# Kernel optimization log

Measured on AMD Instinct MI355X. Metric: run time of the kernel, lower is better.

Reference implementation:

```python
import jax, jax.numpy as jnp
import numpy as np

EPS = 1e-3  # denominator regularizer for weighted mean/cov
DIST_SCALE = 10.0  # raw_call applies 10.0 * distsq before exp weighting

V, K, C, F = 100000, 40, 3, 32


def setup_inputs() -> dict:
    key = jax.random.key(0)
    k1, k2, k3, k4 = jax.random.split(key, 4)
    coordinates = jax.random.normal(k1, (V, C), dtype=jnp.float32)
    distsq = jax.random.uniform(k2, (V, K), dtype=jnp.float32)  # squared distances >= 0
    features = jax.random.uniform(k3, (V, F), dtype=jnp.float32)  # non-negative activations
    n_idxs = jax.random.randint(k4, (V, K), 0, V, dtype=jnp.int32)
    return {"coordinates": coordinates, "distsq": distsq, "features": features, "n_idxs": n_idxs}


def reference(coordinates, distsq, features, n_idxs):
    nV, nC = coordinates.shape
    nF = features.shape[1]
    # SelectWithDefault semantics: index -1 -> default 0
    valid = (n_idxs >= 0)
    idx = jnp.where(valid, n_idxs, 0)
    n_coords = jnp.where(valid[..., None], coordinates[idx], 0.0)  # V x K x C
    w = jnp.exp(-DIST_SCALE * distsq)  # V x K distance weights
    n_feat = jnp.where(valid[..., None], features[idx], 0.0) * w[..., None]  # V x K x F (feature weights)
    wsum = jnp.sum(n_feat, axis=1)  # V x F
    denom = wsum[:, :, None] + EPS  # V x F x 1
    # weighted first moment -> means, weighted second moment -> covariance
    means = jnp.einsum('vkf,vkc->vfc', n_feat, n_coords) / denom  # V x F x C
    second = jnp.einsum('vkf,vkc,vkd->vfcd', n_feat, n_coords, n_coords) / denom[..., None]  # V x F x C x C
    cov = second - means[:, :, :, None] * means[:, :, None, :]  # centered covariance
    out = jnp.concatenate([cov.reshape(nV, nF * nC * nC), means.reshape(nV, nF * nC)], axis=-1)
    return out
```

## Files before the change

### kernel.cpp

```cpp
#include <hip/hip_runtime.h>


constexpr int K = 40;
constexpr int C = 3;
constexpr int F = 32;
constexpr int FH = 16;
constexpr float EPS = 1e-3f;
constexpr float DIST_SCALE = 10.0f;
constexpr int OUT_PER_V = F * C * C + F * C;
constexpr int VPB = 16;
constexpr int PAIRS = VPB * K;
constexpr int WSTRIDE = K + 1;
constexpr int STAGE_F4 = VPB * 48;

typedef float    floatx4 __attribute__((ext_vector_type(4)));
typedef float    f32x8   __attribute__((ext_vector_type(8)));
typedef _Float16 f16x8   __attribute__((ext_vector_type(8)));

__global__ __launch_bounds__(256) void cvt_kernel(
    const float* __restrict__ in, _Float16* __restrict__ lo,
    _Float16* __restrict__ hi, int n4)
{
    const int i = blockIdx.x * 256 + threadIdx.x;
    if (i >= n4) return;
    const int v = i >> 2, q = i & 3;
    const f32x8 x = __builtin_nontemporal_load((const f32x8*)in + i);
    const f16x8 o = __builtin_convertvector(x, f16x8);
    _Float16* dst = (q < 2 ? lo : hi) + (size_t)v * FH + (q & 1) * 8;
    *(f16x8*)dst = o;
}

__global__ __launch_bounds__(256) void neighcov_split(
    const float* __restrict__ coords,
    const float* __restrict__ distsq,
    const _Float16* __restrict__ plane_lo,
    const _Float16* __restrict__ plane_hi,
    const int*   __restrict__ nidx,
    float* __restrict__ out,
    int V)
{
    __shared__ float4  s_wxyz[VPB * WSTRIDE];
    __shared__ int     s_joff[PAIRS];
    __shared__ floatx4 s_stage[STAGE_F4];

    const int tid   = threadIdx.x;
    const int vbase = blockIdx.x * VPB;
    const long long total_pairs = (long long)V * K;

    for (int p = tid; p < PAIRS; p += 256) {
        const long long gp = (long long)vbase * K + p;
        int idx = -1;
        float d = 0.f;
        if (gp < total_pairs) {
            idx = __builtin_nontemporal_load(nidx + gp);
            d   = __builtin_nontemporal_load(distsq + gp);
        }
        const bool valid = (idx >= 0);
        const int j = valid ? idx : 0;
        const float w = valid ? __expf(-DIST_SCALE * d) : 0.f;
        const float x = coords[(size_t)j * 3 + 0];
        const float y = coords[(size_t)j * 3 + 1];
        const float z = coords[(size_t)j * 3 + 2];
        const int vloc = p / K, k = p - vloc * K;
        s_wxyz[vloc * WSTRIDE + k] = make_float4(w, x, y, z);
        s_joff[p] = j * FH;
    }
    __syncthreads();

    const int fl   = tid & 15;
    const int vloc = tid >> 4;
    const float4* wp = &s_wxyz[vloc * WSTRIDE];
    const int*    jp = &s_joff[vloc * K];
    const int rem_v = V - vbase;
    floatx4* o4 = (floatx4*)(out + (size_t)vbase * OUT_PER_V);

    #pragma unroll
    for (int half = 0; half < 2; ++half) {
        const _Float16* __restrict__ plane = half ? plane_hi : plane_lo;

        float wsum = 0.f;
        float m0 = 0.f, m1 = 0.f, m2 = 0.f;
        float s00 = 0.f, s01 = 0.f, s02 = 0.f, s11 = 0.f, s12 = 0.f, s22 = 0.f;

        #pragma unroll 8
        for (int k = 0; k < K; ++k) {
            const float4 q = wp[k];
            const int jo   = jp[k];
            const float feat = (float)plane[jo + fl];
            const float fw = q.x * feat;
            const float x = q.y, y = q.z, z = q.w;
            const float fx = fw * x, fy = fw * y, fz = fw * z;
            wsum += fw;
            m0 += fx;        m1 += fy;        m2 += fz;
            s00 += fx * x;   s01 += fx * y;   s02 += fx * z;
            s11 += fy * y;   s12 += fy * z;   s22 += fz * z;
        }

        const float inv = 1.f / (wsum + EPS);
        const float mu0 = m0 * inv, mu1 = m1 * inv, mu2 = m2 * inv;
        const float c00 = s00 * inv - mu0 * mu0;
        const float c01 = s01 * inv - mu0 * mu1;
        const float c02 = s02 * inv - mu0 * mu2;
        const float c11 = s11 * inv - mu1 * mu1;
        const float c12 = s12 * inv - mu1 * mu2;
        const float c22 = s22 * inv - mu2 * mu2;

        float* s_out = (float*)s_stage;
        float* so = s_out + vloc * 192 + fl * 9;
        so[0] = c00; so[1] = c01; so[2] = c02;
        so[3] = c01; so[4] = c11; so[5] = c12;
        so[6] = c02; so[7] = c12; so[8] = c22;
        float* sm = s_out + vloc * 192 + 144 + fl * 3;
        sm[0] = mu0; sm[1] = mu1; sm[2] = mu2;

        __syncthreads();

        #pragma unroll
        for (int g = tid; g < STAGE_F4; g += 256) {
            const int v = g / 48;
            const int r = g - v * 48;
            if (v < rem_v) {
                const int dst = v * 96 + (r < 36 ? half * 36 + r
                                                 : 72 + half * 12 + (r - 36));
                __builtin_nontemporal_store(s_stage[g], o4 + dst);
            }
        }

        __syncthreads();
    }
}

constexpr int VPB8 = 8;
constexpr int PAIRS8 = VPB8 * K;
constexpr int OUT_F4_8 = VPB8 * OUT_PER_V / 4;

__global__ __launch_bounds__(256) void neighcov_f32(
    const float* __restrict__ coords, const float* __restrict__ distsq,
    const float* __restrict__ features, const int* __restrict__ nidx,
    float* __restrict__ out, int V)
{
    __shared__ float4  s_wxyz[PAIRS8];
    __shared__ int     s_joff[PAIRS8];
    __shared__ floatx4 s_out4[OUT_F4_8];

    const int tid   = threadIdx.x;
    const int vbase = blockIdx.x * VPB8;
    const long long total_pairs = (long long)V * K;

    #pragma unroll
    for (int p = tid; p < PAIRS8; p += 256) {
        const long long gp = (long long)vbase * K + p;
        int idx = -1; float d = 0.f;
        if (gp < total_pairs) {
            idx = __builtin_nontemporal_load(nidx + gp);
            d   = __builtin_nontemporal_load(distsq + gp);
        }
        const bool valid = (idx >= 0);
        const int j = valid ? idx : 0;
        const float w = valid ? __expf(-DIST_SCALE * d) : 0.f;
        s_wxyz[p] = make_float4(w, coords[(size_t)j * 3 + 0],
                                coords[(size_t)j * 3 + 1], coords[(size_t)j * 3 + 2]);
        s_joff[p] = j * F;
    }
    __syncthreads();

    const int f = tid & (F - 1), vloc = tid >> 5;
    const float4* wp = &s_wxyz[vloc * K];
    const int*    jp = &s_joff[vloc * K];

    float wsum = 0.f, m0 = 0.f, m1 = 0.f, m2 = 0.f;
    float s00 = 0.f, s01 = 0.f, s02 = 0.f, s11 = 0.f, s12 = 0.f, s22 = 0.f;
    #pragma unroll 8
    for (int k = 0; k < K; ++k) {
        const float4 q = wp[k];
        const float feat = features[jp[k] + f];
        const float fw = q.x * feat;
        const float x = q.y, y = q.z, z = q.w;
        const float fx = fw * x, fy = fw * y, fz = fw * z;
        wsum += fw; m0 += fx; m1 += fy; m2 += fz;
        s00 += fx * x; s01 += fx * y; s02 += fx * z;
        s11 += fy * y; s12 += fy * z; s22 += fz * z;
    }
    const float inv = 1.f / (wsum + EPS);
    const float mu0 = m0 * inv, mu1 = m1 * inv, mu2 = m2 * inv;
    float* s_out = (float*)s_out4;
    float* so = s_out + vloc * OUT_PER_V + f * 9;
    so[0] = s00 * inv - mu0 * mu0; so[1] = s01 * inv - mu0 * mu1;
    so[2] = s02 * inv - mu0 * mu2; so[3] = so[1];
    so[4] = s11 * inv - mu1 * mu1; so[5] = s12 * inv - mu1 * mu2;
    so[6] = so[2]; so[7] = so[5]; so[8] = s22 * inv - mu2 * mu2;
    float* sm = s_out + vloc * OUT_PER_V + F * 9 + f * 3;
    sm[0] = mu0; sm[1] = mu1; sm[2] = mu2;
    __syncthreads();

    const int rem_v = V - vbase;
    const int lim_f4 = (rem_v >= VPB8) ? OUT_F4_8 : rem_v * (OUT_PER_V / 4);
    floatx4* o4 = (floatx4*)(out + (size_t)vbase * OUT_PER_V);
    #pragma unroll
    for (int g = tid; g < OUT_F4_8; g += 256)
        if (g < lim_f4) __builtin_nontemporal_store(s_out4[g], o4 + g);
}

extern "C" void kernel_launch(void* const* d_in, const int* in_sizes, int n_in,
                              void* d_out, int out_size, void* d_ws, size_t ws_size,
                              hipStream_t stream) {
    const float* coords   = (const float*)d_in[0];
    const float* distsq   = (const float*)d_in[1];
    const float* features = (const float*)d_in[2];
    const int*   nidx     = (const int*)d_in[3];
    float* out = (float*)d_out;

    const int V = in_sizes[0] / C;

    const size_t plane_bytes = (size_t)V * FH * sizeof(_Float16);
    if (ws_size >= 2 * plane_bytes) {
        _Float16* lo = (_Float16*)d_ws;
        _Float16* hi = lo + (size_t)V * FH;
        const int n4 = V * 4;
        cvt_kernel<<<(n4 + 255) / 256, 256, 0, stream>>>(features, lo, hi, n4);
        const int blocks = (V + VPB - 1) / VPB;
        neighcov_split<<<blocks, 256, 0, stream>>>(
            coords, distsq, lo, hi, nidx, out, V);
    } else {
        const int blocks = (V + VPB8 - 1) / VPB8;
        neighcov_f32<<<blocks, 256, 0, stream>>>(
            coords, distsq, features, nidx, out, V);
    }
}
```

Before: 271.6 us.

## Split feature halves across XCDs so each L2 caches one half-plane

Each block now processes one feature half, chosen from the block's XCD (assuming round-robin block-to-XCD dispatch), so XCDs 0-3 gather from the low fp16 plane and 4-7 from the high plane. This aims to cut the L2 working set of the random feature gathers per XCD. In exchange, the neighbor index/distance/coordinate setup and exp are duplicated for both halves. The staging buffer stride is also padded to reduce LDS bank conflicts.

Result: slower. 283.9 us (+4.5%).

```diff
diff --git a/kernel.cpp b/kernel.cpp
--- a/kernel.cpp
+++ b/kernel.cpp
@@ -11,7 +11,7 @@
 constexpr int VPB = 16;
 constexpr int PAIRS = VPB * K;
 constexpr int WSTRIDE = K + 1;
-constexpr int STAGE_F4 = VPB * 48;
+constexpr int VSTRIDE4 = 49;
 
 typedef float    floatx4 __attribute__((ext_vector_type(4)));
 typedef float    f32x8   __attribute__((ext_vector_type(8)));
@@ -30,21 +30,27 @@
     *(f16x8*)dst = o;
 }
 
-__global__ __launch_bounds__(256) void neighcov_split(
+__global__ __launch_bounds__(256) void neighcov_xcd(
     const float* __restrict__ coords,
     const float* __restrict__ distsq,
     const _Float16* __restrict__ plane_lo,
     const _Float16* __restrict__ plane_hi,
     const int*   __restrict__ nidx,
     float* __restrict__ out,
-    int V)
+    int V, int nchunks)
 {
     __shared__ float4  s_wxyz[VPB * WSTRIDE];
     __shared__ int     s_joff[PAIRS];
-    __shared__ floatx4 s_stage[STAGE_F4];
-
-    const int tid   = threadIdx.x;
-    const int vbase = blockIdx.x * VPB;
+    __shared__ floatx4 s_stage[VPB * VSTRIDE4];
+
+    const int b    = blockIdx.x;
+    const int xcd  = b & 7;
+    const int half = xcd >> 2;
+    const int ord  = (b >> 3) * 4 + (xcd & 3);
+    if (ord >= nchunks) return;
+    const int vbase = ord * VPB;
+
+    const int tid = threadIdx.x;
     const long long total_pairs = (long long)V * K;
 
     for (int p = tid; p < PAIRS; p += 256) {
@@ -71,62 +77,56 @@
     const int vloc = tid >> 4;
     const float4* wp = &s_wxyz[vloc * WSTRIDE];
     const int*    jp = &s_joff[vloc * K];
+    const _Float16* __restrict__ plane = half ? plane_hi : plane_lo;
+
+    float wsum = 0.f;
+    float m0 = 0.f, m1 = 0.f, m2 = 0.f;
+    float s00 = 0.f, s01 = 0.f, s02 = 0.f, s11 = 0.f, s12 = 0.f, s22 = 0.f;
+
+    #pragma unroll 8
+    for (int k = 0; k < K; ++k) {
+        const float4 q = wp[k];
+        const int jo   = jp[k];
+        const float feat = (float)plane[jo + fl];
+        const float fw = q.x * feat;
+        const float x = q.y, y = q.z, z = q.w;
+        const float fx = fw * x, fy = fw * y, fz = fw * z;
+        wsum += fw;
+        m0 += fx;        m1 += fy;        m2 += fz;
+        s00 += fx * x;   s01 += fx * y;   s02 += fx * z;
+        s11 += fy * y;   s12 += fy * z;   s22 += fz * z;
+    }
+
+    const float inv = 1.f / (wsum + EPS);
+    const float mu0 = m0 * inv, mu1 = m1 * inv, mu2 = m2 * inv;
+    const float c00 = s00 * inv - mu0 * mu0;
+    const float c01 = s01 * inv - mu0 * mu1;
+    const float c02 = s02 * inv - mu0 * mu2;
+    const float c11 = s11 * inv - mu1 * mu1;
+    const float c12 = s12 * inv - mu1 * mu2;
+    const float c22 = s22 * inv - mu2 * mu2;
+
+    float* s_out = (float*)s_stage;
+    float* so = s_out + vloc * (VSTRIDE4 * 4) + fl * 9;
+    so[0] = c00; so[1] = c01; so[2] = c02;
+    so[3] = c01; so[4] = c11; so[5] = c12;
+    so[6] = c02; so[7] = c12; so[8] = c22;
+    float* sm = s_out + vloc * (VSTRIDE4 * 4) + 144 + fl * 3;
+    sm[0] = mu0; sm[1] = mu1; sm[2] = mu2;
+
+    __syncthreads();
+
     const int rem_v = V - vbase;
     floatx4* o4 = (floatx4*)(out + (size_t)vbase * OUT_PER_V);
-
     #pragma unroll
-    for (int half = 0; half < 2; ++half) {
-        const _Float16* __restrict__ plane = half ? plane_hi : plane_lo;
-
-        float wsum = 0.f;
-        float m0 = 0.f, m1 = 0.f, m2 = 0.f;
-        float s00 = 0.f, s01 = 0.f, s02 = 0.f, s11 = 0.f, s12 = 0.f, s22 = 0.f;
-
-        #pragma unroll 8
-        for (int k = 0; k < K; ++k) {
-            const float4 q = wp[k];
-            const int jo   = jp[k];
-            const float feat = (float)plane[jo + fl];
-            const float fw = q.x * feat;
-            const float x = q.y, y = q.z, z = q.w;
-            const float fx = fw * x, fy = fw * y, fz = fw * z;
-            wsum += fw;
-            m0 += fx;        m1 += fy;        m2 += fz;
-            s00 += fx * x;   s01 += fx * y;   s02 += fx * z;
-            s11 += fy * y;   s12 += fy * z;   s22 += fz * z;
+    for (int g = tid; g < VPB * 48; g += 256) {
+        const int v = g / 48;
+        const int r = g - v * 48;
+        if (v < rem_v) {
+            const int dst = v * 96 + (r < 36 ? half * 36 + r
+                                             : 72 + half * 12 + (r - 36));
+            __builtin_nontemporal_store(s_stage[v * VSTRIDE4 + r], o4 + dst);
         }
-
-        const float inv = 1.f / (wsum + EPS);
-        const float mu0 = m0 * inv, mu1 = m1 * inv, mu2 = m2 * inv;
-        const float c00 = s00 * inv - mu0 * mu0;
-        const float c01 = s01 * inv - mu0 * mu1;
-        const float c02 = s02 * inv - mu0 * mu2;
-        const float c11 = s11 * inv - mu1 * mu1;
-        const float c12 = s12 * inv - mu1 * mu2;
-        const float c22 = s22 * inv - mu2 * mu2;
-
-        float* s_out = (float*)s_stage;
-        float* so = s_out + vloc * 192 + fl * 9;
-        so[0] = c00; so[1] = c01; so[2] = c02;
-        so[3] = c01; so[4] = c11; so[5] = c12;
-        so[6] = c02; so[7] = c12; so[8] = c22;
-        float* sm = s_out + vloc * 192 + 144 + fl * 3;
-        sm[0] = mu0; sm[1] = mu1; sm[2] = mu2;
-
-        __syncthreads();
-
-        #pragma unroll
-        for (int g = tid; g < STAGE_F4; g += 256) {
-            const int v = g / 48;
-            const int r = g - v * 48;
-            if (v < rem_v) {
-                const int dst = v * 96 + (r < 36 ? half * 36 + r
-                                                 : 72 + half * 12 + (r - 36));
-                __builtin_nontemporal_store(s_stage[g], o4 + dst);
-            }
-        }
-
-        __syncthreads();
     }
 }
 
@@ -218,9 +218,10 @@
         _Float16* hi = lo + (size_t)V * FH;
         const int n4 = V * 4;
         cvt_kernel<<<(n4 + 255) / 256, 256, 0, stream>>>(features, lo, hi, n4);
-        const int blocks = (V + VPB - 1) / VPB;
-        neighcov_split<<<blocks, 256, 0, stream>>>(
-            coords, distsq, lo, hi, nidx, out, V);
+        const int nchunks = (V + VPB - 1) / VPB;
+        const int grid = 8 * ((nchunks + 3) / 4);
+        neighcov_xcd<<<grid, 256, 0, stream>>>(
+            coords, distsq, lo, hi, nidx, out, V, nchunks);
     } else {
         const int blocks = (V + VPB8 - 1) / VPB8;
         neighcov_f32<<<blocks, 256, 0, stream>>>(
```

## Use single fp16 feature array with each thread handling two features per neighbor

Applied to the files above, without the earlier changes.

Replaces the two half-width fp16 feature planes with one contiguous fp16 array. Each of 16 threads per vertex now loads an f16x2 pair and accumulates statistics for two features in one pass over the neighbors, so the shared weight and coordinate reads and the gather index loop happen once instead of twice. The output is staged in two 8-vertex chunks written contiguously. The cost is doubled accumulator register pressure, a 32-byte row gather per neighbor, and divergent staging writes.

Measured after the change: 274.2 us. Within noise of the previous version (+1.0%).

```diff
diff --git a/kernel.cpp b/kernel.cpp
--- a/kernel.cpp
+++ b/kernel.cpp
@@ -4,44 +4,41 @@
 constexpr int K = 40;
 constexpr int C = 3;
 constexpr int F = 32;
-constexpr int FH = 16;
 constexpr float EPS = 1e-3f;
 constexpr float DIST_SCALE = 10.0f;
 constexpr int OUT_PER_V = F * C * C + F * C;
 constexpr int VPB = 16;
 constexpr int PAIRS = VPB * K;
 constexpr int WSTRIDE = K + 1;
-constexpr int STAGE_F4 = VPB * 48;
+constexpr int OUT_F4 = 768;
 
 typedef float    floatx4 __attribute__((ext_vector_type(4)));
 typedef float    f32x8   __attribute__((ext_vector_type(8)));
 typedef _Float16 f16x8   __attribute__((ext_vector_type(8)));
+typedef _Float16 f16x2   __attribute__((ext_vector_type(2)));
 
 __global__ __launch_bounds__(256) void cvt_kernel(
-    const float* __restrict__ in, _Float16* __restrict__ lo,
-    _Float16* __restrict__ hi, int n4)
+    const float* __restrict__ in, _Float16* __restrict__ out16, int n8)
 {
     const int i = blockIdx.x * 256 + threadIdx.x;
-    if (i >= n4) return;
-    const int v = i >> 2, q = i & 3;
-    const f32x8 x = __builtin_nontemporal_load((const f32x8*)in + i);
-    const f16x8 o = __builtin_convertvector(x, f16x8);
-    _Float16* dst = (q < 2 ? lo : hi) + (size_t)v * FH + (q & 1) * 8;
-    *(f16x8*)dst = o;
-}
-
-__global__ __launch_bounds__(256) void neighcov_split(
+    if (i < n8) {
+        const f32x8 v = __builtin_nontemporal_load((const f32x8*)in + i);
+        const f16x8 o = __builtin_convertvector(v, f16x8);
+        *((f16x8*)out16 + i) = o;
+    }
+}
+
+__global__ __launch_bounds__(256) void neighcov_f16x2(
     const float* __restrict__ coords,
     const float* __restrict__ distsq,
-    const _Float16* __restrict__ plane_lo,
-    const _Float16* __restrict__ plane_hi,
+    const _Float16* __restrict__ features,
     const int*   __restrict__ nidx,
     float* __restrict__ out,
     int V)
 {
     __shared__ float4  s_wxyz[VPB * WSTRIDE];
     __shared__ int     s_joff[PAIRS];
-    __shared__ floatx4 s_stage[STAGE_F4];
+    __shared__ floatx4 s_out4[OUT_F4];
 
     const int tid   = threadIdx.x;
     const int vbase = blockIdx.x * VPB;
@@ -61,9 +58,9 @@
         const float x = coords[(size_t)j * 3 + 0];
         const float y = coords[(size_t)j * 3 + 1];
         const float z = coords[(size_t)j * 3 + 2];
-        const int vloc = p / K, k = p - vloc * K;
-        s_wxyz[vloc * WSTRIDE + k] = make_float4(w, x, y, z);
-        s_joff[p] = j * FH;
+        const int vl = p / K, kk = p - vl * K;
+        s_wxyz[vl * WSTRIDE + kk] = make_float4(w, x, y, z);
+        s_joff[p] = j * F;
     }
     __syncthreads();
 
@@ -71,61 +68,76 @@
     const int vloc = tid >> 4;
     const float4* wp = &s_wxyz[vloc * WSTRIDE];
     const int*    jp = &s_joff[vloc * K];
-    const int rem_v = V - vbase;
-    floatx4* o4 = (floatx4*)(out + (size_t)vbase * OUT_PER_V);
-
+
+    float wsA = 0.f, m0A = 0.f, m1A = 0.f, m2A = 0.f;
+    float s00A = 0.f, s01A = 0.f, s02A = 0.f, s11A = 0.f, s12A = 0.f, s22A = 0.f;
+    float wsB = 0.f, m0B = 0.f, m1B = 0.f, m2B = 0.f;
+    float s00B = 0.f, s01B = 0.f, s02B = 0.f, s11B = 0.f, s12B = 0.f, s22B = 0.f;
+
+    #pragma unroll 8
+    for (int k = 0; k < K; ++k) {
+        const float4 q = wp[k];
+        const int jo   = jp[k];
+        const f16x2 f2 = *(const f16x2*)(features + jo + 2 * fl);
+        const float x = q.y, y = q.z, z = q.w;
+        const float ftA = (float)f2.x, ftB = (float)f2.y;
+        const float fwA = q.x * ftA,   fwB = q.x * ftB;
+        const float fxA = fwA * x, fyA = fwA * y, fzA = fwA * z;
+        const float fxB = fwB * x, fyB = fwB * y, fzB = fwB * z;
+        wsA += fwA;  m0A += fxA;  m1A += fyA;  m2A += fzA;
+        s00A += fxA * x; s01A += fxA * y; s02A += fxA * z;
+        s11A += fyA * y; s12A += fyA * z; s22A += fzA * z;
+        wsB += fwB;  m0B += fxB;  m1B += fyB;  m2B += fzB;
+        s00B += fxB * x; s01B += fxB * y; s02B += fxB * z;
+        s11B += fyB * y; s12B += fyB * z; s22B += fzB * z;
+    }
+
+    const float invA = 1.f / (wsA + EPS);
+    const float muA0 = m0A * invA, muA1 = m1A * invA, muA2 = m2A * invA;
+    const float cA00 = s00A * invA - muA0 * muA0;
+    const float cA01 = s01A * invA - muA0 * muA1;
+    const float cA02 = s02A * invA - muA0 * muA2;
+    const float cA11 = s11A * invA - muA1 * muA1;
+    const float cA12 = s12A * invA - muA1 * muA2;
+    const float cA22 = s22A * invA - muA2 * muA2;
+
+    const float invB = 1.f / (wsB + EPS);
+    const float muB0 = m0B * invB, muB1 = m1B * invB, muB2 = m2B * invB;
+    const float cB00 = s00B * invB - muB0 * muB0;
+    const float cB01 = s01B * invB - muB0 * muB1;
+    const float cB02 = s02B * invB - muB0 * muB2;
+    const float cB11 = s11B * invB - muB1 * muB1;
+    const float cB12 = s12B * invB - muB1 * muB2;
+    const float cB22 = s22B * invB - muB2 * muB2;
+
+    float* s_out = (float*)s_out4;
     #pragma unroll
-    for (int half = 0; half < 2; ++half) {
-        const _Float16* __restrict__ plane = half ? plane_hi : plane_lo;
-
-        float wsum = 0.f;
-        float m0 = 0.f, m1 = 0.f, m2 = 0.f;
-        float s00 = 0.f, s01 = 0.f, s02 = 0.f, s11 = 0.f, s12 = 0.f, s22 = 0.f;
-
-        #pragma unroll 8
-        for (int k = 0; k < K; ++k) {
-            const float4 q = wp[k];
-            const int jo   = jp[k];
-            const float feat = (float)plane[jo + fl];
-            const float fw = q.x * feat;
-            const float x = q.y, y = q.z, z = q.w;
-            const float fx = fw * x, fy = fw * y, fz = fw * z;
-            wsum += fw;
-            m0 += fx;        m1 += fy;        m2 += fz;
-            s00 += fx * x;   s01 += fx * y;   s02 += fx * z;
-            s11 += fy * y;   s12 += fy * z;   s22 += fz * z;
-        }
-
-        const float inv = 1.f / (wsum + EPS);
-        const float mu0 = m0 * inv, mu1 = m1 * inv, mu2 = m2 * inv;
-        const float c00 = s00 * inv - mu0 * mu0;
-        const float c01 = s01 * inv - mu0 * mu1;
-        const float c02 = s02 * inv - mu0 * mu2;
-        const float c11 = s11 * inv - mu1 * mu1;
-        const float c12 = s12 * inv - mu1 * mu2;
-        const float c22 = s22 * inv - mu2 * mu2;
-
-        float* s_out = (float*)s_stage;
-        float* so = s_out + vloc * 192 + fl * 9;
-        so[0] = c00; so[1] = c01; so[2] = c02;
-        so[3] = c01; so[4] = c11; so[5] = c12;
-        so[6] = c02; so[7] = c12; so[8] = c22;
-        float* sm = s_out + vloc * 192 + 144 + fl * 3;
-        sm[0] = mu0; sm[1] = mu1; sm[2] = mu2;
-
+    for (int c = 0; c < 2; ++c) {
+        if ((vloc >> 3) == c) {
+            const int vl = vloc & 7;
+            float* so = s_out + vl * OUT_PER_V + (2 * fl) * 9;
+            so[0]  = cA00; so[1]  = cA01; so[2]  = cA02;
+            so[3]  = cA01; so[4]  = cA11; so[5]  = cA12;
+            so[6]  = cA02; so[7]  = cA12; so[8]  = cA22;
+            so[9]  = cB00; so[10] = cB01; so[11] = cB02;
+            so[12] = cB01; so[13] = cB11; so[14] = cB12;
+            so[15] = cB02; so[16] = cB12; so[17] = cB22;
+            float* sm = s_out + vl * OUT_PER_V + F * 9 + (2 * fl) * 3;
+            sm[0] = muA0; sm[1] = muA1; sm[2] = muA2;
+            sm[3] = muB0; sm[4] = muB1; sm[5] = muB2;
+        }
         __syncthreads();
 
+        const int vb    = vbase + c * 8;
+        const int rem_v = V - vb;
+        const int lim   = (rem_v >= 8 ? 8 : (rem_v > 0 ? rem_v : 0)) * 96;
+        floatx4* o4 = (floatx4*)(out + (size_t)vb * OUT_PER_V);
         #pragma unroll
-        for (int g = tid; g < STAGE_F4; g += 256) {
-            const int v = g / 48;
-            const int r = g - v * 48;
-            if (v < rem_v) {
-                const int dst = v * 96 + (r < 36 ? half * 36 + r
-                                                 : 72 + half * 12 + (r - 36));
-                __builtin_nontemporal_store(s_stage[g], o4 + dst);
+        for (int g = tid; g < OUT_F4; g += 256) {
+            if (g < lim) {
+                __builtin_nontemporal_store(s_out4[g], o4 + g);
             }
         }
-
         __syncthreads();
     }
 }
@@ -212,15 +224,15 @@
 
     const int V = in_sizes[0] / C;
 
-    const size_t plane_bytes = (size_t)V * FH * sizeof(_Float16);
-    if (ws_size >= 2 * plane_bytes) {
-        _Float16* lo = (_Float16*)d_ws;
-        _Float16* hi = lo + (size_t)V * FH;
-        const int n4 = V * 4;
-        cvt_kernel<<<(n4 + 255) / 256, 256, 0, stream>>>(features, lo, hi, n4);
+    const size_t need = (size_t)V * F * sizeof(_Float16);
+    const int nelem = V * F;
+    if (ws_size >= need && (nelem & 7) == 0) {
+        _Float16* feat16 = (_Float16*)d_ws;
+        const int n8 = nelem / 8;
+        cvt_kernel<<<(n8 + 255) / 256, 256, 0, stream>>>(features, feat16, n8);
         const int blocks = (V + VPB - 1) / VPB;
-        neighcov_split<<<blocks, 256, 0, stream>>>(
-            coords, distsq, lo, hi, nidx, out, V);
+        neighcov_f16x2<<<blocks, 256, 0, stream>>>(
+            coords, distsq, feat16, nidx, out, V);
     } else {
         const int blocks = (V + VPB8 - 1) / VPB8;
         neighcov_f32<<<blocks, 256, 0, stream>>>(
```
